# Kernel optimization log

Hardware: AMD Instinct MI355X
Metric: run time of the kernel (lower is better)

## Reference

```python
import jax, jax.numpy as jnp
import numpy as np

B, T, D, V, L = 128, 1024, 512, 128, 128
BLANK = V - 1          # keras ctc_batch_cost uses num_classes-1 as blank
EPS = 1e-7             # tf.keras.backend.epsilon()
NEG = jnp.float32(-1e30)


def setup_inputs() -> dict:
    key = jax.random.key(0)
    k1, k2, k3, k4 = jax.random.split(key, 4)
    x = jax.random.normal(k1, (B, T, D), jnp.float32)
    W = jax.random.normal(k2, (D, V), jnp.float32) / np.sqrt(D)
    b = jnp.zeros((V,), jnp.float32)
    targets = jax.random.randint(k3, (B, L), 0, V - 1, dtype=jnp.int32)   # labels in [0, V-2]
    targets_length = jax.random.randint(k4, (B,), 16, L + 1, dtype=jnp.int32)  # >=1
    return {"x": x, "W": W, "b": b, "targets": targets, "targets_length": targets_length}


def _ctc_neg_log_lik(log_probs, targets, targets_length):
    # log_probs: [B,T,V]; targets: [B,L]; returns per-example -log p(targets | probs)
    Bb, Tt, Vv = log_probs.shape
    Ll = targets.shape[1]
    S = 2 * Ll + 1
    # extended label sequence: blank, l1, blank, l2, ..., blank   [B,S]
    ext = jnp.full((Bb, S), BLANK, dtype=targets.dtype)
    ext = ext.at[:, 1::2].set(targets)
    # allow skip transition s-2 -> s when ext[s] != blank and ext[s] != ext[s-2]
    ext2 = jnp.concatenate([jnp.full((Bb, 2), -1, ext.dtype), ext[:, :-2]], axis=1)
    allow2 = (ext != BLANK) & (ext != ext2)                       # [B,S]

    def emit(logp_t):  # logp_t [B,V] -> [B,S]
        return jnp.take_along_axis(logp_t, ext, axis=1)

    # t = 0: only s=0 (blank) and s=1 (first label) reachable
    e0 = emit(log_probs[:, 0])
    alpha0 = jnp.where(jnp.arange(S)[None, :] < 2, e0, NEG)       # [B,S]

    def step(alpha, logp_t):
        a1 = jnp.concatenate([jnp.full((Bb, 1), NEG), alpha[:, :-1]], axis=1)
        a2 = jnp.concatenate([jnp.full((Bb, 2), NEG), alpha[:, :-2]], axis=1)
        m = jnp.logaddexp(alpha, a1)
        m = jnp.where(allow2, jnp.logaddexp(m, a2), m)
        return m + emit(logp_t), None

    alpha_T, _ = jax.lax.scan(step, alpha0, jnp.swapaxes(log_probs, 0, 1)[1:])
    # final states: s = 2*len (trailing blank) and s = 2*len - 1 (last label)
    last = 2 * targets_length                                     # [B]
    aN = jnp.take_along_axis(alpha_T, last[:, None], axis=1)[:, 0]
    aN1 = jnp.take_along_axis(alpha_T, (last - 1)[:, None], axis=1)[:, 0]
    return -jnp.logaddexp(aN, aN1)                                # [B]


def reference(x, W, b, targets, targets_length):
    # Dense -> Softmax (module outputs probabilities) -> ctc_batch_cost: log(p + eps) -> CTC DP -> sum
    probs = jax.nn.softmax(jnp.einsum("btd,dv->btv", x, W) + b, axis=-1)
    log_probs = jnp.log(probs + EPS)
    loss = _ctc_neg_log_lik(log_probs, targets, targets_length)
    return jnp.sum(loss)
```

## Files before the change

### kernel.cpp

```cpp
#include <hip/hip_runtime.h>

#define Bb 128
#define Tt 1024
#define Dd 512
#define Vv 128
#define Ll 128
#define EPSF 1e-7f
#define PADK 72
#define NEGF -1e30f

typedef float f4 __attribute__((ext_vector_type(4)));
typedef short s8 __attribute__((ext_vector_type(8)));
typedef float f32x4 __attribute__((ext_vector_type(4)));

__device__ inline unsigned int f2bf(float f) {
    unsigned int u = __float_as_uint(f);
    return (u + 0x7fffu + ((u >> 16) & 1u)) >> 16;
}

__device__ inline float lae2(float x, float y) {
    float m = fmaxf(x, y);
    float d = fminf(x, y) - m;
    return m + __logf(1.f + __expf(d));
}

__device__ inline float dpp_shr1(float v) {
    return __int_as_float(__builtin_amdgcn_update_dpp(
        0, __float_as_int(v), 0x138, 0xf, 0xf, false));
}
__device__ inline int dpp_shr1_i(int v) {
    return __builtin_amdgcn_update_dpp(0, v, 0x138, 0xf, 0xf, false);
}

__global__ void wt_kernel(const float* __restrict__ W, unsigned short* __restrict__ Wt) {
    int idx = blockIdx.x * 256 + threadIdx.x;
    int v = idx >> 9, k = idx & 511;
    Wt[idx] = (unsigned short)f2bf(W[k * Vv + v]);
}

__global__ __launch_bounds__(256) void gemm_softmax(
    const float* __restrict__ x, const unsigned short* __restrict__ Wt,
    const float* __restrict__ bias, float* __restrict__ LP)
{
    __shared__ __align__(16) char smem[73728];
    __shared__ __align__(16) float invs[128];
    unsigned short* Al0 = (unsigned short*)smem;
    unsigned short* Al1 = (unsigned short*)(smem + 18432);
    unsigned short* Bl0 = (unsigned short*)(smem + 36864);
    unsigned short* Bl1 = (unsigned short*)(smem + 55296);
    float* lds = (float*)smem;

    const int tid = threadIdx.x;
    const int wave = tid >> 6, lane = tid & 63;
    const int lm = lane & 15, lq = lane >> 4;
    const int wm = (wave >> 1) << 6, wn = (wave & 1) << 6;
    const long row0 = (long)blockIdx.x << 7;

    f32x4 acc[4][4];
    #pragma unroll
    for (int i = 0; i < 4; i++)
        #pragma unroll
        for (int j = 0; j < 4; j++)
            acc[i][j] = (f32x4){0.f, 0.f, 0.f, 0.f};

    f4 ra[8], rb[4];

#define STAGE_REGS(K0) do {                                                 \
    int kb_ = (K0) << 6;                                                    \
    _Pragma("unroll")                                                       \
    for (int i = 0; i < 8; i++) {                                           \
        int idx = tid + (i << 8);                                           \
        int r = idx >> 4, c4 = idx & 15;                                    \
        ra[i] = *(const f4*)(x + (row0 + r) * Dd + kb_ + (c4 << 2));        \
    }                                                                       \
    _Pragma("unroll")                                                       \
    for (int i = 0; i < 4; i++) {                                           \
        int idx = tid + (i << 8);                                           \
        int vr = idx >> 3, c = idx & 7;                                     \
        rb[i] = *(const f4*)(Wt + vr * 512 + kb_ + (c << 3));               \
    } } while (0)

#define WRITE_LDS(AL, BL) do {                                              \
    _Pragma("unroll")                                                       \
    for (int i = 0; i < 8; i++) {                                           \
        int idx = tid + (i << 8);                                           \
        int r = idx >> 4, c4 = idx & 15;                                    \
        unsigned int lo_, hi_;                                              \
        asm("v_cvt_pk_bf16_f32 %0, %1, %2" : "=v"(lo_)                      \
            : "v"(ra[i].x), "v"(ra[i].y));                                  \
        asm("v_cvt_pk_bf16_f32 %0, %1, %2" : "=v"(hi_)                      \
            : "v"(ra[i].z), "v"(ra[i].w));                                  \
        unsigned long long q_ = (unsigned long long)lo_                     \
                              | ((unsigned long long)hi_ << 32);            \
        *(unsigned long long*)((AL) + r * PADK + (c4 << 2)) = q_;           \
    }                                                                       \
    _Pragma("unroll")                                                       \
    for (int i = 0; i < 4; i++) {                                           \
        int idx = tid + (i << 8);                                           \
        int vr = idx >> 3, c = idx & 7;                                     \
        *(f4*)((BL) + vr * PADK + (c << 3)) = rb[i];                        \
    } } while (0)

#define MFMA_TILE(AL, BL) do {                                              \
    _Pragma("unroll")                                                       \
    for (int kk = 0; kk < 64; kk += 32) {                                   \
        s8 afr[4], bfr[4];                                                  \
        _Pragma("unroll")                                                   \
        for (int mi = 0; mi < 4; mi++)                                      \
            afr[mi] = *(const s8*)((AL) + (wm + (mi << 4) + lm) * PADK      \
                                    + kk + (lq << 3));                      \
        _Pragma("unroll")                                                   \
        for (int ni = 0; ni < 4; ni++)                                      \
            bfr[ni] = *(const s8*)((BL) + (wn + (ni << 4) + lm) * PADK      \
                                    + kk + (lq << 3));                      \
        _Pragma("unroll")                                                   \
        for (int mi = 0; mi < 4; mi++)                                      \
            _Pragma("unroll")                                               \
            for (int ni = 0; ni < 4; ni++)                                  \
                acc[mi][ni] = __builtin_amdgcn_mfma_f32_16x16x32_bf16(      \
                    afr[mi], bfr[ni], acc[mi][ni], 0, 0, 0);                \
    } } while (0)

    STAGE_REGS(0);
    WRITE_LDS(Al0, Bl0);
    __syncthreads();
    #pragma unroll
    for (int s = 0; s < 4; s++) {
        STAGE_REGS(2 * s + 1);
        MFMA_TILE(Al0, Bl0);
        WRITE_LDS(Al1, Bl1);
        __syncthreads();
        if (s < 3) STAGE_REGS(2 * s + 2);
        MFMA_TILE(Al1, Bl1);
        if (s < 3) {
            WRITE_LDS(Al0, Bl0);
            __syncthreads();
        }
    }
    __syncthreads();
    #pragma unroll
    for (int mi = 0; mi < 4; mi++) {
        #pragma unroll
        for (int ni = 0; ni < 4; ni++) {
            int col = wn + (ni << 4) + lm;
            float bv = bias[col];
            #pragma unroll
            for (int r = 0; r < 4; r++) {
                int row = wm + (mi << 4) + (lq << 2) + r;
                int word = (row << 7) + ((((col >> 2) ^ ((row >> 2) & 7)) & 31) << 2) + (col & 3);
                lds[word] = acc[mi][ni][r] + bv;
            }
        }
    }
    __syncthreads();
    {
        const int row = tid >> 1, h = tid & 1;
        float m = -1e30f;
        #pragma unroll
        for (int cc = 0; cc < 16; cc++) {
            int word = (row << 7) + (((cc + (h << 4) + row) & 31) << 2);
            f4 v = *(const f4*)(lds + word);
            m = fmaxf(m, fmaxf(fmaxf(v.x, v.y), fmaxf(v.z, v.w)));
        }
        m = fmaxf(m, __shfl_xor(m, 1));
        float s = 0.f;
        #pragma unroll
        for (int cc = 0; cc < 16; cc++) {
            int word = (row << 7) + (((cc + (h << 4) + row) & 31) << 2);
            f4 v = *(f4*)(lds + word);
            v.x = __expf(v.x - m); v.y = __expf(v.y - m);
            v.z = __expf(v.z - m); v.w = __expf(v.w - m);
            s += v.x + v.y + v.z + v.w;
            *(f4*)(lds + word) = v;
        }
        s += __shfl_xor(s, 1);
        if (h == 0) invs[row] = 1.f / s;
    }
    __syncthreads();
    {
        const int l = tid & 31, g = tid >> 5;
        const int bidx = blockIdx.x >> 3;
        const int tbase = (blockIdx.x & 7) << 7;
        const f4 iv = *(const f4*)(invs + (l << 2));
        #pragma unroll
        for (int jj = 0; jj < 16; jj++) {
            const int v = (g << 4) + jj;
            const int swz = ((v >> 2) ^ (l & 7)) << 2;
            const int r0 = v & 3;
            f4 o;
            #pragma unroll
            for (int r = 0; r < 4; r++) {
                int t = (l << 2) + r;
                o[r] = fmaf(lds[(t << 7) + swz + r0], iv[r], EPSF);
            }
            *(f4*)(LP + ((long)bidx * Vv + v) * Tt + tbase + (l << 2)) = o;
        }
    }
#undef STAGE_REGS
#undef WRITE_LDS
#undef MFMA_TILE
}

__global__ __launch_bounds__(64) void ctc_kernel(
    const float* __restrict__ PT, const int* __restrict__ targets,
    const int* __restrict__ tlen, float* __restrict__ out)
{
    const int b = blockIdx.x;
    const int lane = threadIdx.x;
    const float* baseP = PT + (long)b * Vv * Tt;

    const int tgt0 = targets[(b << 7) + (lane << 1)];
    const int tgt1 = targets[(b << 7) + (lane << 1) + 1];
    int tp = __shfl_up(tgt1, 1);
    if (lane == 0) tp = -1;
    const bool mA = (tgt0 != tp);
    const bool mB = (tgt1 != tgt0);
    const float mBf = mB ? 1.f : 0.f;

    const float* pB = baseP + 127 * Tt;
    const float* p0 = baseP + (long)tgt0 * Tt;
    const float* p1 = baseP + (long)tgt1 * Tt;

    float u0 = (lane == 0) ? pB[0] : 0.f;
    float u1 = (lane == 0) ? p0[0] : 0.f;
    float u2 = 0.f, u3 = 0.f, u4 = 0.f;
    int anc = 0;
    float fprev = 1.f;
    float fprevA = mA ? 1.f : 0.f;

    f4 Xb[4], Xs[4], Xt[4], Yb[4], Ys[4], Yt[4], Zb[4], Zs[4], Zt[4];

#define LOADW(BUF, W) do {                                                  \
    int tn_ = ((W) < 63 ? (W) : 63) << 4;                                   \
    _Pragma("unroll")                                                       \
    for (int q = 0; q < 4; q++) {                                           \
        BUF##b[q] = *(const f4*)(pB + tn_ + (q << 2));                      \
        BUF##s[q] = *(const f4*)(p0 + tn_ + (q << 2));                      \
        BUF##t[q] = *(const f4*)(p1 + tn_ + (q << 2));                      \
    } } while (0)

#define DOSTEP(BUF, i) do {                                                 \
    float lb = BUF##b[(i) >> 2][(i) & 3];                                   \
    float l0 = BUF##s[(i) >> 2][(i) & 3];                                   \
    float l1 = BUF##t[(i) >> 2][(i) & 3];                                   \
    float s_ = dpp_shr1(u3);                                \
    float t01 = u0 + u1;                                                    \
    float n0 = fmaf(s_, fprev,  u0) * lb;                                   \
    float n1 = fmaf(s_, fprevA, t01) * l0;                                  \
    float n2 = (u1 + u2) * lb;                                              \
    float n3 = fmaf(u1, mBf, u2 + u3) * l1;                                 \
    float n4 = (u3 + u4) * lb;                                              \
    u0 = n0; u1 = n1; u2 = n2; u3 = n3; u4 = n4; } while (0)

#define RESCALE(ADOPT) do {                                                 \
    float umax = fmaxf(fmaxf(fmaxf(u0, u1), fmaxf(u2, u3)), u4);            \
    int e = (int)((__float_as_uint(umax) >> 23) & 0xffu) - 126;             \
    float sc = __uint_as_float((unsigned)(127 - e) << 23);        \
    u0 *= sc; u1 *= sc; u2 *= sc; u3 *= sc; u4 *= sc;       \
    if (ADOPT) {                                                            \
        bool live = umax > 0.f;                                             \
        anc = live ? (anc + e) : anc;                                       \
        _Pragma("unroll")                                                   \
        for (int r_ = 0; r_ < 3; r_++) {                                    \
            int cp_ = dpp_shr1_i(anc);                                      \
            anc = live ? anc : cp_;                                         \
        }                                                                   \
    } else {                                                                \
        anc += e;                                                           \
    }                                                                       \
    int cp = dpp_shr1_i(anc);                                               \
    int d_ = cp - anc;                                                      \
    d_ = d_ > 96 ? 96 : d_;                     \
    fprev = (d_ < -126) ? 0.f                                               \
           : __uint_as_float((unsigned)((d_ + 127) << 23));                 \
    fprevA = mA ? fprev : 0.f; } while (0)

#define WINDOW(CUR, N2, W, ADOPT, ISTART) do {                              \
    LOADW(N2, (W) + 2);                                                     \
    _Pragma("unroll")                                                       \
    for (int i = ISTART; i < 16; i++) {                                     \
        DOSTEP(CUR, i);                                                     \
        if ((i & 3) == 3) RESCALE(ADOPT);                                   \
    } } while (0)

    LOADW(X, 0);
    LOADW(Y, 1);
    WINDOW(X, Z, 0, true, 1);
    for (int g = 0; g < 5; g++) {
        int w = 1 + 3 * g;
        WINDOW(Y, X, w,     true, 0);
        WINDOW(Z, Y, w + 1, true, 0);
        WINDOW(X, Z, w + 2, true, 0);
    }
    for (int g = 0; g < 16; g++) {
        int w = 16 + 3 * g;
        WINDOW(Y, X, w,     false, 0);
        WINDOW(Z, Y, w + 1, false, 0);
        WINDOW(X, Z, w + 2, false, 0);
    }

    __shared__ float af[257];
    const float LN2 = 0.69314718056f;
    float fa = (float)anc;
    af[(lane << 2) + 0] = u0 > 0.f ? (fa + log2f(u0)) * LN2 : NEGF;
    af[(lane << 2) + 1] = u1 > 0.f ? (fa + log2f(u1)) * LN2 : NEGF;
    af[(lane << 2) + 2] = u2 > 0.f ? (fa + log2f(u2)) * LN2 : NEGF;
    af[(lane << 2) + 3] = u3 > 0.f ? (fa + log2f(u3)) * LN2 : NEGF;
    if (lane == 63) af[256] = u4 > 0.f ? (fa + log2f(u4)) * LN2 : NEGF;
    __syncthreads();
    if (lane == 0) {
        int len = tlen[b];
        float loss = -lae2(af[2 * len], af[2 * len - 1]);
        atomicAdd(out, loss);
    }
}

extern "C" void kernel_launch(void* const* d_in, const int* in_sizes, int n_in,
                              void* d_out, int out_size, void* d_ws, size_t ws_size,
                              hipStream_t stream) {
    const float* x       = (const float*)d_in[0];
    const float* W       = (const float*)d_in[1];
    const float* bias    = (const float*)d_in[2];
    const int*   targets = (const int*)d_in[3];
    const int*   tl      = (const int*)d_in[4];
    float* out = (float*)d_out;

    float* LP = (float*)d_ws;
    unsigned short* Wt = (unsigned short*)((char*)d_ws + (size_t)Bb * Tt * Vv * 4);

    (void)hipMemsetAsync(out, 0, sizeof(float), stream);
    wt_kernel<<<256, 256, 0, stream>>>(W, Wt);
    gemm_softmax<<<1024, 256, 0, stream>>>(x, Wt, bias, LP);
    ctc_kernel<<<Bb, 64, 0, stream>>>(LP, targets, tl, out);
}
```

Baseline: 442.2 us.

## Stream fp32 activations straight into LDS and load weight fragments directly into registers

New measurement: 430.5 us. 2.7% less time.

```diff
diff --git a/kernel.cpp b/kernel.cpp
--- a/kernel.cpp
+++ b/kernel.cpp
@@ -6,11 +6,11 @@
 #define Vv 128
 #define Ll 128
 #define EPSF 1e-7f
-#define PADK 72
 #define NEGF -1e30f
 
 typedef float f4 __attribute__((ext_vector_type(4)));
 typedef short s8 __attribute__((ext_vector_type(8)));
+typedef unsigned int u32x4 __attribute__((ext_vector_type(4)));
 typedef float f32x4 __attribute__((ext_vector_type(4)));
 
 __device__ inline unsigned int f2bf(float f) {
@@ -42,13 +42,9 @@
     const float* __restrict__ x, const unsigned short* __restrict__ Wt,
     const float* __restrict__ bias, float* __restrict__ LP)
 {
-    __shared__ __align__(16) char smem[73728];
+    __shared__ __align__(16) float Abuf[2][8192];
     __shared__ __align__(16) float invs[128];
-    unsigned short* Al0 = (unsigned short*)smem;
-    unsigned short* Al1 = (unsigned short*)(smem + 18432);
-    unsigned short* Bl0 = (unsigned short*)(smem + 36864);
-    unsigned short* Bl1 = (unsigned short*)(smem + 55296);
-    float* lds = (float*)smem;
+    float* lds = &Abuf[0][0];
 
     const int tid = threadIdx.x;
     const int wave = tid >> 6, lane = tid & 63;
@@ -63,81 +59,80 @@
         for (int j = 0; j < 4; j++)
             acc[i][j] = (f32x4){0.f, 0.f, 0.f, 0.f};
 
-    f4 ra[8], rb[4];
-
-#define STAGE_REGS(K0) do {                                                 \
-    int kb_ = (K0) << 6;                                                    \
+    s8 breg[2][2][4];
+
+#define STAGE(BUF, K0) do {                                                 \
     _Pragma("unroll")                                                       \
     for (int i = 0; i < 8; i++) {                                           \
-        int idx = tid + (i << 8);                                           \
-        int r = idx >> 4, c4 = idx & 15;                                    \
-        ra[i] = *(const f4*)(x + (row0 + r) * Dd + kb_ + (c4 << 2));        \
-    }                                                                       \
-    _Pragma("unroll")                                                       \
-    for (int i = 0; i < 4; i++) {                                           \
-        int idx = tid + (i << 8);                                           \
-        int vr = idx >> 3, c = idx & 7;                                     \
-        rb[i] = *(const f4*)(Wt + vr * 512 + kb_ + (c << 3));               \
+        int r_ = (wave << 5) + (i << 2) + (lane >> 4);                      \
+        int c_ = (lane & 15) ^ (r_ & 15);                                   \
+        const float* gsrc = x + (row0 + r_) * Dd + (K0) + (c_ << 2);        \
+        float* ldst = &(BUF)[(wave << 11) + (i << 8)];                      \
+        __builtin_amdgcn_global_load_lds(                                   \
+            (const __attribute__((address_space(1))) unsigned int*)gsrc,    \
+            (__attribute__((address_space(3))) unsigned int*)ldst,          \
+            16, 0, 0);                                                      \
     } } while (0)
 
-#define WRITE_LDS(AL, BL) do {                                              \
-    _Pragma("unroll")                                                       \
-    for (int i = 0; i < 8; i++) {                                           \
-        int idx = tid + (i << 8);                                           \
-        int r = idx >> 4, c4 = idx & 15;                                    \
-        unsigned int lo_, hi_;                                              \
-        asm("v_cvt_pk_bf16_f32 %0, %1, %2" : "=v"(lo_)                      \
-            : "v"(ra[i].x), "v"(ra[i].y));                                  \
-        asm("v_cvt_pk_bf16_f32 %0, %1, %2" : "=v"(hi_)                      \
-            : "v"(ra[i].z), "v"(ra[i].w));                                  \
-        unsigned long long q_ = (unsigned long long)lo_                     \
-                              | ((unsigned long long)hi_ << 32);            \
-        *(unsigned long long*)((AL) + r * PADK + (c4 << 2)) = q_;           \
-    }                                                                       \
-    _Pragma("unroll")                                                       \
-    for (int i = 0; i < 4; i++) {                                           \
-        int idx = tid + (i << 8);                                           \
-        int vr = idx >> 3, c = idx & 7;                                     \
-        *(f4*)((BL) + vr * PADK + (c << 3)) = rb[i];                        \
-    } } while (0)
-
-#define MFMA_TILE(AL, BL) do {                                              \
-    _Pragma("unroll")                                                       \
-    for (int kk = 0; kk < 64; kk += 32) {                                   \
-        s8 afr[4], bfr[4];                                                  \
-        _Pragma("unroll")                                                   \
-        for (int mi = 0; mi < 4; mi++)                                      \
-            afr[mi] = *(const s8*)((AL) + (wm + (mi << 4) + lm) * PADK      \
-                                    + kk + (lq << 3));                      \
+#define LOADB(TB, K0) do {                                                  \
+    _Pragma("unroll")                                                       \
+    for (int kx = 0; kx < 2; kx++)                                          \
         _Pragma("unroll")                                                   \
         for (int ni = 0; ni < 4; ni++)                                      \
-            bfr[ni] = *(const s8*)((BL) + (wn + (ni << 4) + lm) * PADK      \
-                                    + kk + (lq << 3));                      \
+            breg[TB][kx][ni] = *(const s8*)(Wt + (wn + (ni << 4) + lm) * 512 \
+                                            + (K0) + (kx << 5) + (lq << 3)); \
+    } while (0)
+
+#define COMPUTE(BUF, TB) do {                                               \
+    _Pragma("unroll")                                                       \
+    for (int kx = 0; kx < 2; kx++) {                                        \
+        s8 afr[4];                                                          \
+        _Pragma("unroll")                                                   \
+        for (int mi = 0; mi < 4; mi++) {                                    \
+            int r_ = wm + (mi << 4) + lm;                                   \
+            int c0_ = (kx << 3) + (lq << 1);                                \
+            f4 lo = *(const f4*)&(BUF)[(r_ << 6) + ((c0_ ^ (r_ & 15)) << 2)]; \
+            f4 hi = *(const f4*)&(BUF)[(r_ << 6) + (((c0_ + 1) ^ (r_ & 15)) << 2)]; \
+            unsigned int w0_, w1_, w2_, w3_;                                \
+            asm("v_cvt_pk_bf16_f32 %0, %1, %2" : "=v"(w0_) : "v"(lo.x), "v"(lo.y)); \
+            asm("v_cvt_pk_bf16_f32 %0, %1, %2" : "=v"(w1_) : "v"(lo.z), "v"(lo.w)); \
+            asm("v_cvt_pk_bf16_f32 %0, %1, %2" : "=v"(w2_) : "v"(hi.x), "v"(hi.y)); \
+            asm("v_cvt_pk_bf16_f32 %0, %1, %2" : "=v"(w3_) : "v"(hi.z), "v"(hi.w)); \
+            union { u32x4 u; s8 s; } cv_;                                   \
+            cv_.u = (u32x4){w0_, w1_, w2_, w3_};                            \
+            afr[mi] = cv_.s;                                                \
+        }                                                                   \
         _Pragma("unroll")                                                   \
         for (int mi = 0; mi < 4; mi++)                                      \
             _Pragma("unroll")                                               \
             for (int ni = 0; ni < 4; ni++)                                  \
                 acc[mi][ni] = __builtin_amdgcn_mfma_f32_16x16x32_bf16(      \
-                    afr[mi], bfr[ni], acc[mi][ni], 0, 0, 0);                \
+                    afr[mi], breg[TB][kx][ni], acc[mi][ni], 0, 0, 0);       \
     } } while (0)
 
-    STAGE_REGS(0);
-    WRITE_LDS(Al0, Bl0);
-    __syncthreads();
+    STAGE(Abuf[0], 0);
+    LOADB(0, 0);
+    asm volatile("s_waitcnt vmcnt(0)");
+    __builtin_amdgcn_sched_barrier(0);
+    __builtin_amdgcn_s_barrier();
+
     #pragma unroll
-    for (int s = 0; s < 4; s++) {
-        STAGE_REGS(2 * s + 1);
-        MFMA_TILE(Al0, Bl0);
-        WRITE_LDS(Al1, Bl1);
-        __syncthreads();
-        if (s < 3) STAGE_REGS(2 * s + 2);
-        MFMA_TILE(Al1, Bl1);
-        if (s < 3) {
-            WRITE_LDS(Al0, Bl0);
-            __syncthreads();
-        }
-    }
-    __syncthreads();
+    for (int t = 0; t < 8; t++) {
+        if (t < 7) {
+            STAGE(Abuf[(t + 1) & 1], (t + 1) << 6);
+            LOADB((t + 1) & 1, (t + 1) << 6);
+            asm volatile("s_waitcnt vmcnt(16)");
+        } else {
+            asm volatile("s_waitcnt vmcnt(0)");
+        }
+        __builtin_amdgcn_sched_barrier(0);
+        COMPUTE(Abuf[t & 1], t & 1);
+        __builtin_amdgcn_s_barrier();
+    }
+#undef STAGE
+#undef LOADB
+#undef COMPUTE
+
     #pragma unroll
     for (int mi = 0; mi < 4; mi++) {
         #pragma unroll
@@ -196,9 +191,6 @@
             *(f4*)(LP + ((long)bidx * Vv + v) * Tt + tbase + (l << 2)) = o;
         }
     }
-#undef STAGE_REGS
-#undef WRITE_LDS
-#undef MFMA_TILE
 }
 
 __global__ __launch_bounds__(64) void ctc_kernel(
```
